# Kernel tuning notes

Hardware: AMD Instinct MI355X
Metric: run time of the kernel (lower is better)

The kernel has to match this reference:

```python
import jax, jax.numpy as jnp
import numpy as np

NUM_NODES = 200000
NUM_EDGES = 200000
NUM_GRAPHS = 2048
F_IN = 128
H = 64


def setup_inputs() -> dict:
    key = jax.random.key(0)
    ks = jax.random.split(key, 16)
    x = jax.random.normal(ks[0], (NUM_NODES, F_IN), dtype=jnp.float32)
    edge_index = jax.random.randint(ks[1], (2, NUM_EDGES), 0, NUM_NODES, dtype=jnp.int64)
    batch = jnp.sort(jax.random.randint(ks[2], (NUM_NODES,), 0, NUM_GRAPHS, dtype=jnp.int64))
    s_in = 1.0 / np.sqrt(F_IN)
    s_h = 1.0 / np.sqrt(H)
    W1a = jax.random.uniform(ks[3], (F_IN, H), jnp.float32, -s_in, s_in)
    b1a = jax.random.uniform(ks[4], (H,), jnp.float32, -s_in, s_in)
    W1b = jax.random.uniform(ks[5], (H, H), jnp.float32, -s_h, s_h)
    b1b = jax.random.uniform(ks[6], (H,), jnp.float32, -s_h, s_h)
    W2a = jax.random.uniform(ks[7], (H, H), jnp.float32, -s_h, s_h)
    b2a = jax.random.uniform(ks[8], (H,), jnp.float32, -s_h, s_h)
    W2b = jax.random.uniform(ks[9], (H, H), jnp.float32, -s_h, s_h)
    b2b = jax.random.uniform(ks[10], (H,), jnp.float32, -s_h, s_h)
    fcW = jax.random.uniform(ks[11], (H, 1), jnp.float32, -s_h, s_h)
    fcb = jax.random.uniform(ks[12], (1,), jnp.float32, -s_h, s_h)
    return {"x": x, "edge_index": edge_index, "batch": batch,
            "W1a": W1a, "b1a": b1a, "W1b": W1b, "b1b": b1b,
            "W2a": W2a, "b2a": b2a, "W2b": W2b, "b2b": b2b,
            "fcW": fcW, "fcb": fcb}


def gin_conv(h, edge_index, Wa, ba, Wb, bb):
    # sum aggregation: messages from source (row 0) scattered to target (row 1)
    msgs = h[edge_index[0]]  # [E, D]
    agg = jax.ops.segment_sum(msgs, edge_index[1], num_segments=NUM_NODES)
    z = h + agg  # eps = 0 default: (1+eps)*x + sum_j x_j
    z = jnp.maximum(z @ Wa + ba, 0.0)
    return z @ Wb + bb


def reference(x, edge_index, batch, W1a, b1a, W1b, b1b, W2a, b2a, W2b, b2b, fcW, fcb):
    h = jnp.maximum(gin_conv(x, edge_index, W1a, b1a, W1b, b1b), 0.0)
    h = jnp.maximum(gin_conv(h, edge_index, W2a, b2a, W2b, b2b), 0.0)
    # global mean pool per graph
    sums = jax.ops.segment_sum(h, batch, num_segments=NUM_GRAPHS)  # [G, H]
    counts = jax.ops.segment_sum(jnp.ones((h.shape[0],), h.dtype), batch, num_segments=NUM_GRAPHS)
    pooled = sums / jnp.maximum(counts, 1.0)[:, None]
    out = pooled @ fcW + fcb  # [G, 1]
    return out.squeeze(-1)
```

## Files before the change

kernel.cpp:

```cpp
#include <hip/hip_runtime.h>
#include <hip/hip_bf16.h>


#define NODES 200000
#define NPAD  200064
#define EDGES 200000
#define GRAPHS 2048
#define NB_SCAN 782

typedef __attribute__((ext_vector_type(8))) short short8;
typedef __attribute__((ext_vector_type(4))) float f32x4;

__device__ __forceinline__ unsigned short f2bf(float f) {
    unsigned u = __builtin_bit_cast(unsigned, f);
    u = (u + 0x7fffu + ((u >> 16) & 1u)) >> 16;
    return (unsigned short)u;
}
__device__ __forceinline__ float bf2f(unsigned short h) {
    unsigned u = ((unsigned)h) << 16;
    return __builtin_bit_cast(float, u);
}

__device__ __forceinline__ void wconv(const float* __restrict__ W,
                                      short* __restrict__ F, int e, int NE)
{
    int lane = e & 63, nb = (e >> 6) & 3, kc = e >> 8;
    int col = nb * 16 + (lane & 15);
    int kb = kc * 32 + ((lane >> 4) * 8);
    short8 hi, lo;
    #pragma unroll
    for (int j = 0; j < 8; ++j) {
        float w = W[(size_t)(kb + j) * 64 + col];
        unsigned short h = f2bf(w);
        float r = w - bf2f(h);
        hi[j] = (short)h;
        lo[j] = (short)f2bf(r);
    }
    *reinterpret_cast<short8*>(F + (size_t)e * 8) = hi;
    *reinterpret_cast<short8*>(F + (size_t)NE * 8 + (size_t)e * 8) = lo;
}

__global__ __launch_bounds__(256) void setup_k(
    const float* __restrict__ W1a, const float* __restrict__ W1b,
    const float* __restrict__ W2a, const float* __restrict__ W2b,
    short* __restrict__ F1a, short* __restrict__ F1b,
    short* __restrict__ F2a, short* __restrict__ F2b,
    int* __restrict__ cnt, float* __restrict__ gacc)
{
    int t = blockIdx.x * 256 + threadIdx.x;
    if (t < NODES) cnt[t] = 0;
    if (t < GRAPHS) gacc[t] = 0.f;
    if (t < 1024)      wconv(W1a, F1a, t, 1024);
    else if (t < 1536) wconv(W1b, F1b, t - 1024, 512);
    else if (t < 2048) wconv(W2a, F2a, t - 1536, 512);
    else if (t < 2560) wconv(W2b, F2b, t - 2048, 512);
}

__global__ __launch_bounds__(256) void count_k(
    const int* __restrict__ ei, int* __restrict__ cnt, int E)
{
    int e = blockIdx.x * 256 + threadIdx.x;
    if (e < E) atomicAdd(&cnt[ei[E + e]], 1);
}

__global__ __launch_bounds__(256) void scan1_k(
    const int* __restrict__ cnt, int* __restrict__ excl,
    int* __restrict__ bsum, int N)
{
    __shared__ int sh[256];
    int tid = threadIdx.x;
    int i = blockIdx.x * 256 + tid;
    int v = (i < N) ? cnt[i] : 0;
    sh[tid] = v;
    __syncthreads();
    for (int off = 1; off < 256; off <<= 1) {
        int t = (tid >= off) ? sh[tid - off] : 0;
        __syncthreads();
        sh[tid] += t;
        __syncthreads();
    }
    if (i < N) excl[i] = sh[tid] - v;
    if (tid == 255) bsum[blockIdx.x] = sh[255];
}

__global__ __launch_bounds__(256) void scan23_k(
    int* __restrict__ rowptr, const int* __restrict__ bsum,
    int* __restrict__ cursor, int N, int E)
{
    __shared__ int wsum[4];
    __shared__ int soff;
    int tid = threadIdx.x;
    int partial = 0;
    for (int b = tid; b < blockIdx.x; b += 256) partial += bsum[b];
    #pragma unroll
    for (int off = 32; off >= 1; off >>= 1) partial += __shfl_down(partial, off);
    if ((tid & 63) == 0) wsum[tid >> 6] = partial;
    __syncthreads();
    if (tid == 0) soff = wsum[0] + wsum[1] + wsum[2] + wsum[3];
    __syncthreads();
    int i = blockIdx.x * 256 + tid;
    if (i < N) {
        int v = rowptr[i] + soff;
        rowptr[i] = v;
        cursor[i] = v;
    }
    if (i == 0) rowptr[N] = E;
}

__global__ __launch_bounds__(256) void fill_k(
    const int* __restrict__ ei, int* __restrict__ cursor,
    int* __restrict__ srcs, int E)
{
    int e = blockIdx.x * 256 + threadIdx.x;
    if (e < E) {
        int d = ei[E + e];
        int p = atomicAdd(&cursor[d], 1);
        srcs[p] = ei[e];
    }
}

__device__ __forceinline__ void cvt_a8(const float4& a, const float4& b,
                                       short8& hi, short8& lo)
{
    float av[8] = {a.x, a.y, a.z, a.w, b.x, b.y, b.z, b.w};
    #pragma unroll
    for (int j = 0; j < 8; ++j) {
        unsigned short h = f2bf(av[j]);
        float r = av[j] - bf2f(h);
        hi[j] = (short)h;
        lo[j] = (short)f2bf(r);
    }
}

__global__ __launch_bounds__(256) void mm1_k(
    const float* __restrict__ A, const short* __restrict__ Wf,
    float* __restrict__ out, int N)
{
    const int tid = threadIdx.x;
    const int lane = tid & 63;
    const int wv = tid >> 6;
    const int row0w = blockIdx.x * 128 + wv * 32;
    const int grp = lane >> 4, c = lane & 15;
    const int koff = grp * 8;

    const float* Ar0 = A + (size_t)min(row0w + c, N - 1) * 128;
    const float* Ar1 = A + (size_t)min(row0w + 16 + c, N - 1) * 128;

    f32x4 acc[2][4];
    #pragma unroll
    for (int rg = 0; rg < 2; ++rg)
        #pragma unroll
        for (int nb = 0; nb < 4; ++nb)
            acc[rg][nb] = (f32x4){0.f, 0.f, 0.f, 0.f};

    #pragma unroll
    for (int kc = 0; kc < 4; ++kc) {
        const int kb = kc * 32 + koff;
        float4 a00 = *reinterpret_cast<const float4*>(Ar0 + kb);
        float4 a01 = *reinterpret_cast<const float4*>(Ar0 + kb + 4);
        float4 a10 = *reinterpret_cast<const float4*>(Ar1 + kb);
        float4 a11 = *reinterpret_cast<const float4*>(Ar1 + kb + 4);
        short8 h0, l0, h1, l1;
        cvt_a8(a00, a01, h0, l0);
        cvt_a8(a10, a11, h1, l1);
        #pragma unroll
        for (int nb = 0; nb < 4; ++nb) {
            short8 whi = *reinterpret_cast<const short8*>(Wf + ((size_t)((kc * 4 + nb) * 64) + lane) * 8);
            short8 wlo = *reinterpret_cast<const short8*>(Wf + ((size_t)(1024 + (kc * 4 + nb) * 64) + lane) * 8);
            acc[0][nb] = __builtin_amdgcn_mfma_f32_16x16x32_bf16(h0, whi, acc[0][nb], 0, 0, 0);
            acc[0][nb] = __builtin_amdgcn_mfma_f32_16x16x32_bf16(l0, whi, acc[0][nb], 0, 0, 0);
            acc[0][nb] = __builtin_amdgcn_mfma_f32_16x16x32_bf16(h0, wlo, acc[0][nb], 0, 0, 0);
            acc[1][nb] = __builtin_amdgcn_mfma_f32_16x16x32_bf16(h1, whi, acc[1][nb], 0, 0, 0);
            acc[1][nb] = __builtin_amdgcn_mfma_f32_16x16x32_bf16(l1, whi, acc[1][nb], 0, 0, 0);
            acc[1][nb] = __builtin_amdgcn_mfma_f32_16x16x32_bf16(h1, wlo, acc[1][nb], 0, 0, 0);
        }
    }

    #pragma unroll
    for (int rg = 0; rg < 2; ++rg)
        #pragma unroll
        for (int nb = 0; nb < 4; ++nb)
            #pragma unroll
            for (int reg = 0; reg < 4; ++reg)
                out[(size_t)(row0w + rg * 16 + grp * 4 + reg) * 64 + nb * 16 + c] = acc[rg][nb][reg];
}

__device__ __forceinline__ void agg_frag16(
    const float* __restrict__ y, const int* __restrict__ rowptr,
    const int* __restrict__ srcs, const float* __restrict__ bias,
    int n, int koff, bool valid, short8 fh[2], short8 fl[2])
{
    if (!valid) {
        #pragma unroll
        for (int i = 0; i < 8; ++i) {
            fh[0][i] = 0; fl[0][i] = 0; fh[1][i] = 0; fl[1][i] = 0;
        }
        return;
    }
    float a[16];
    {
        const float* yr = y + (size_t)n * 64;
        float4 a0 = *reinterpret_cast<const float4*>(yr + koff);
        float4 a1 = *reinterpret_cast<const float4*>(yr + koff + 4);
        float4 a2 = *reinterpret_cast<const float4*>(yr + 32 + koff);
        float4 a3 = *reinterpret_cast<const float4*>(yr + 32 + koff + 4);
        float4 b0 = *reinterpret_cast<const float4*>(bias + koff);
        float4 b1 = *reinterpret_cast<const float4*>(bias + koff + 4);
        float4 b2 = *reinterpret_cast<const float4*>(bias + 32 + koff);
        float4 b3 = *reinterpret_cast<const float4*>(bias + 32 + koff + 4);
        a[0] = a0.x + b0.x;  a[1] = a0.y + b0.y;  a[2] = a0.z + b0.z;  a[3] = a0.w + b0.w;
        a[4] = a1.x + b1.x;  a[5] = a1.y + b1.y;  a[6] = a1.z + b1.z;  a[7] = a1.w + b1.w;
        a[8] = a2.x + b2.x;  a[9] = a2.y + b2.y;  a[10] = a2.z + b2.z; a[11] = a2.w + b2.w;
        a[12] = a3.x + b3.x; a[13] = a3.y + b3.y; a[14] = a3.z + b3.z; a[15] = a3.w + b3.w;
    }
    int s0 = rowptr[n], s1 = rowptr[n + 1];
    int j = s0;
    for (; j + 2 <= s1; j += 2) {
        const float* ysA = y + (size_t)srcs[j] * 64;
        const float* ysB = y + (size_t)srcs[j + 1] * 64;
        float4 A0 = *reinterpret_cast<const float4*>(ysA + koff);
        float4 A1 = *reinterpret_cast<const float4*>(ysA + koff + 4);
        float4 A2 = *reinterpret_cast<const float4*>(ysA + 32 + koff);
        float4 A3 = *reinterpret_cast<const float4*>(ysA + 32 + koff + 4);
        float4 B0 = *reinterpret_cast<const float4*>(ysB + koff);
        float4 B1 = *reinterpret_cast<const float4*>(ysB + koff + 4);
        float4 B2 = *reinterpret_cast<const float4*>(ysB + 32 + koff);
        float4 B3 = *reinterpret_cast<const float4*>(ysB + 32 + koff + 4);
        a[0] += A0.x;  a[1] += A0.y;  a[2] += A0.z;  a[3] += A0.w;
        a[4] += A1.x;  a[5] += A1.y;  a[6] += A1.z;  a[7] += A1.w;
        a[8] += A2.x;  a[9] += A2.y;  a[10] += A2.z; a[11] += A2.w;
        a[12] += A3.x; a[13] += A3.y; a[14] += A3.z; a[15] += A3.w;
        a[0] += B0.x;  a[1] += B0.y;  a[2] += B0.z;  a[3] += B0.w;
        a[4] += B1.x;  a[5] += B1.y;  a[6] += B1.z;  a[7] += B1.w;
        a[8] += B2.x;  a[9] += B2.y;  a[10] += B2.z; a[11] += B2.w;
        a[12] += B3.x; a[13] += B3.y; a[14] += B3.z; a[15] += B3.w;
    }
    if (j < s1) {
        const float* ys = y + (size_t)srcs[j] * 64;
        float4 v0 = *reinterpret_cast<const float4*>(ys + koff);
        float4 v1 = *reinterpret_cast<const float4*>(ys + koff + 4);
        float4 v2 = *reinterpret_cast<const float4*>(ys + 32 + koff);
        float4 v3 = *reinterpret_cast<const float4*>(ys + 32 + koff + 4);
        a[0] += v0.x;  a[1] += v0.y;  a[2] += v0.z;  a[3] += v0.w;
        a[4] += v1.x;  a[5] += v1.y;  a[6] += v1.z;  a[7] += v1.w;
        a[8] += v2.x;  a[9] += v2.y;  a[10] += v2.z; a[11] += v2.w;
        a[12] += v3.x; a[13] += v3.y; a[14] += v3.z; a[15] += v3.w;
    }
    #pragma unroll
    for (int i = 0; i < 16; ++i) {
        float v = fmaxf(a[i], 0.f);
        unsigned short h = f2bf(v);
        float r = v - bf2f(h);
        fh[i >> 3][i & 7] = (short)h;
        fl[i >> 3][i & 7] = (short)f2bf(r);
    }
}

__global__ __launch_bounds__(256) void mmaggmm_k(
    const float* __restrict__ y, const int* __restrict__ rowptr,
    const int* __restrict__ srcs, const float* __restrict__ bagg,
    const short* __restrict__ Wf1, const float* __restrict__ b1,
    const short* __restrict__ Wf2, float* __restrict__ out, int N)
{
    __shared__ short hT[4][32 * 72];
    __shared__ short lT[4][32 * 72];
    const int tid = threadIdx.x;
    const int lane = tid & 63;
    const int wv = tid >> 6;
    const int row0w = blockIdx.x * 128 + wv * 32;
    const int grp = lane >> 4, c = lane & 15;
    const int koff = grp * 8;

    short8 fh0[2], fl0[2], fh1[2], fl1[2];
    {
        int n0 = row0w + c;
        int n1 = row0w + 16 + c;
        agg_frag16(y, rowptr, srcs, bagg, n0, koff, n0 < N, fh0, fl0);
        agg_frag16(y, rowptr, srcs, bagg, n1, koff, n1 < N, fh1, fl1);
    }

    f32x4 acc[2][4];
    #pragma unroll
    for (int rg = 0; rg < 2; ++rg)
        #pragma unroll
        for (int nb = 0; nb < 4; ++nb)
            acc[rg][nb] = (f32x4){0.f, 0.f, 0.f, 0.f};

    #pragma unroll
    for (int kc = 0; kc < 2; ++kc) {
        #pragma unroll
        for (int nb = 0; nb < 4; ++nb) {
            short8 whi = *reinterpret_cast<const short8*>(Wf1 + ((size_t)((kc * 4 + nb) * 64) + lane) * 8);
            short8 wlo = *reinterpret_cast<const short8*>(Wf1 + ((size_t)(512 + (kc * 4 + nb) * 64) + lane) * 8);
            acc[0][nb] = __builtin_amdgcn_mfma_f32_16x16x32_bf16(fh0[kc], whi, acc[0][nb], 0, 0, 0);
            acc[0][nb] = __builtin_amdgcn_mfma_f32_16x16x32_bf16(fl0[kc], whi, acc[0][nb], 0, 0, 0);
            acc[0][nb] = __builtin_amdgcn_mfma_f32_16x16x32_bf16(fh0[kc], wlo, acc[0][nb], 0, 0, 0);
            acc[1][nb] = __builtin_amdgcn_mfma_f32_16x16x32_bf16(fh1[kc], whi, acc[1][nb], 0, 0, 0);
            acc[1][nb] = __builtin_amdgcn_mfma_f32_16x16x32_bf16(fl1[kc], whi, acc[1][nb], 0, 0, 0);
            acc[1][nb] = __builtin_amdgcn_mfma_f32_16x16x32_bf16(fh1[kc], wlo, acc[1][nb], 0, 0, 0);
        }
    }

    #pragma unroll
    for (int rg = 0; rg < 2; ++rg)
        #pragma unroll
        for (int nb = 0; nb < 4; ++nb) {
            const int col = nb * 16 + c;
            const float bv = b1[col];
            #pragma unroll
            for (int reg = 0; reg < 4; ++reg) {
                const int lr = rg * 16 + grp * 4 + reg;
                float v = fmaxf(acc[rg][nb][reg] + bv, 0.f);
                unsigned short h = f2bf(v);
                float r = v - bf2f(h);
                hT[wv][lr * 72 + col] = (short)h;
                lT[wv][lr * 72 + col] = (short)f2bf(r);
            }
        }
    __syncthreads();

    f32x4 acc2[2][4];
    #pragma unroll
    for (int rg = 0; rg < 2; ++rg)
        #pragma unroll
        for (int nb = 0; nb < 4; ++nb)
            acc2[rg][nb] = (f32x4){0.f, 0.f, 0.f, 0.f};

    #pragma unroll
    for (int kc = 0; kc < 2; ++kc) {
        const int kb = kc * 32 + koff;
        short8 h0 = *reinterpret_cast<const short8*>(&hT[wv][(0 + c) * 72 + kb]);
        short8 l0 = *reinterpret_cast<const short8*>(&lT[wv][(0 + c) * 72 + kb]);
        short8 h1 = *reinterpret_cast<const short8*>(&hT[wv][(16 + c) * 72 + kb]);
        short8 l1 = *reinterpret_cast<const short8*>(&lT[wv][(16 + c) * 72 + kb]);
        #pragma unroll
        for (int nb = 0; nb < 4; ++nb) {
            short8 whi = *reinterpret_cast<const short8*>(Wf2 + ((size_t)((kc * 4 + nb) * 64) + lane) * 8);
            short8 wlo = *reinterpret_cast<const short8*>(Wf2 + ((size_t)(512 + (kc * 4 + nb) * 64) + lane) * 8);
            acc2[0][nb] = __builtin_amdgcn_mfma_f32_16x16x32_bf16(h0, whi, acc2[0][nb], 0, 0, 0);
            acc2[0][nb] = __builtin_amdgcn_mfma_f32_16x16x32_bf16(l0, whi, acc2[0][nb], 0, 0, 0);
            acc2[0][nb] = __builtin_amdgcn_mfma_f32_16x16x32_bf16(h0, wlo, acc2[0][nb], 0, 0, 0);
            acc2[1][nb] = __builtin_amdgcn_mfma_f32_16x16x32_bf16(h1, whi, acc2[1][nb], 0, 0, 0);
            acc2[1][nb] = __builtin_amdgcn_mfma_f32_16x16x32_bf16(l1, whi, acc2[1][nb], 0, 0, 0);
            acc2[1][nb] = __builtin_amdgcn_mfma_f32_16x16x32_bf16(h1, wlo, acc2[1][nb], 0, 0, 0);
        }
    }

    #pragma unroll
    for (int rg = 0; rg < 2; ++rg)
        #pragma unroll
        for (int nb = 0; nb < 4; ++nb)
            #pragma unroll
            for (int reg = 0; reg < 4; ++reg)
                out[(size_t)(row0w + rg * 16 + grp * 4 + reg) * 64 + nb * 16 + c] = acc2[rg][nb][reg];
}

__global__ __launch_bounds__(256) void mmaggpool_k(
    const float* __restrict__ y, const int* __restrict__ rowptr,
    const int* __restrict__ srcs, const float* __restrict__ bagg,
    const short* __restrict__ Wf, const float* __restrict__ bias,
    const float* __restrict__ fcW, const int* __restrict__ batch,
    float* __restrict__ gacc, int N)
{
    __shared__ float rd[4][32];
    __shared__ int bls[4][32];
    const int tid = threadIdx.x;
    const int lane = tid & 63;
    const int wv = tid >> 6;
    const int row0w = blockIdx.x * 128 + wv * 32;
    const int grp = lane >> 4, c = lane & 15;
    const int koff = grp * 8;

    if (lane < 32) bls[wv][lane] = batch[min(row0w + lane, N - 1)];

    short8 fh0[2], fl0[2], fh1[2], fl1[2];
    {
        int n0 = row0w + c;
        int n1 = row0w + 16 + c;
        agg_frag16(y, rowptr, srcs, bagg, n0, koff, n0 < N, fh0, fl0);
        agg_frag16(y, rowptr, srcs, bagg, n1, koff, n1 < N, fh1, fl1);
    }

    f32x4 acc[2][4];
    #pragma unroll
    for (int rg = 0; rg < 2; ++rg)
        #pragma unroll
        for (int nb = 0; nb < 4; ++nb)
            acc[rg][nb] = (f32x4){0.f, 0.f, 0.f, 0.f};

    #pragma unroll
    for (int kc = 0; kc < 2; ++kc) {
        #pragma unroll
        for (int nb = 0; nb < 4; ++nb) {
            short8 whi = *reinterpret_cast<const short8*>(Wf + ((size_t)((kc * 4 + nb) * 64) + lane) * 8);
            short8 wlo = *reinterpret_cast<const short8*>(Wf + ((size_t)(512 + (kc * 4 + nb) * 64) + lane) * 8);
            acc[0][nb] = __builtin_amdgcn_mfma_f32_16x16x32_bf16(fh0[kc], whi, acc[0][nb], 0, 0, 0);
            acc[0][nb] = __builtin_amdgcn_mfma_f32_16x16x32_bf16(fl0[kc], whi, acc[0][nb], 0, 0, 0);
            acc[0][nb] = __builtin_amdgcn_mfma_f32_16x16x32_bf16(fh0[kc], wlo, acc[0][nb], 0, 0, 0);
            acc[1][nb] = __builtin_amdgcn_mfma_f32_16x16x32_bf16(fh1[kc], whi, acc[1][nb], 0, 0, 0);
            acc[1][nb] = __builtin_amdgcn_mfma_f32_16x16x32_bf16(fl1[kc], whi, acc[1][nb], 0, 0, 0);
            acc[1][nb] = __builtin_amdgcn_mfma_f32_16x16x32_bf16(fh1[kc], wlo, acc[1][nb], 0, 0, 0);
        }
    }

    float bv[4], fw[4];
    #pragma unroll
    for (int nb = 0; nb < 4; ++nb) {
        bv[nb] = bias[nb * 16 + c];
        fw[nb] = fcW[nb * 16 + c];
    }

    #pragma unroll
    for (int rg = 0; rg < 2; ++rg)
        #pragma unroll
        for (int reg = 0; reg < 4; ++reg) {
            float t = 0.f;
            #pragma unroll
            for (int nb = 0; nb < 4; ++nb)
                t += fmaxf(acc[rg][nb][reg] + bv[nb], 0.f) * fw[nb];
            t += __shfl_xor(t, 1, 16);
            t += __shfl_xor(t, 2, 16);
            t += __shfl_xor(t, 4, 16);
            t += __shfl_xor(t, 8, 16);
            if (c == 0) rd[wv][rg * 16 + grp * 4 + reg] = t;
        }

    if (lane == 0) {
        int cnt = min(32, N - row0w);
        if (cnt > 0) {
            int curg = bls[wv][0];
            float s = rd[wv][0];
            for (int i = 1; i < cnt; ++i) {
                int g = bls[wv][i];
                float v = rd[wv][i];
                if (g == curg) s += v;
                else { atomicAdd(&gacc[curg], s); curg = g; s = v; }
            }
            atomicAdd(&gacc[curg], s);
        }
    }
}

__global__ __launch_bounds__(256) void finalize_k(
    const float* __restrict__ gacc, const int* __restrict__ batch,
    const float* __restrict__ fcb, float* __restrict__ out, int N, int G)
{
    int g = blockIdx.x * 256 + threadIdx.x;
    if (g >= G) return;
    int lo = 0, hi = N;
    while (lo < hi) { int m = (lo + hi) >> 1; if (batch[m] < g) lo = m + 1; else hi = m; }
    int start = lo;
    hi = N;
    while (lo < hi) { int m = (lo + hi) >> 1; if (batch[m] < g + 1) lo = m + 1; else hi = m; }
    float cnt = fmaxf((float)(lo - start), 1.f);
    out[g] = gacc[g] / cnt + fcb[0];
}

extern "C" void kernel_launch(void* const* d_in, const int* in_sizes, int n_in,
                              void* d_out, int out_size, void* d_ws, size_t ws_size,
                              hipStream_t stream)
{
    const float* x     = (const float*)d_in[0];
    const int*   ei    = (const int*)d_in[1];
    const int*   batch = (const int*)d_in[2];
    const float* W1a   = (const float*)d_in[3];
    const float* b1a   = (const float*)d_in[4];
    const float* W1b   = (const float*)d_in[5];
    const float* b1b   = (const float*)d_in[6];
    const float* W2a   = (const float*)d_in[7];
    const float* b2a   = (const float*)d_in[8];
    const float* W2b   = (const float*)d_in[9];
    const float* b2b   = (const float*)d_in[10];
    const float* fcW   = (const float*)d_in[11];
    const float* fcb   = (const float*)d_in[12];
    float* out = (float*)d_out;

    const int N = NODES, E = EDGES, G = GRAPHS;
    char* ws = (char*)d_ws;

    float* y1 = (float*)ws;
    float* y2 = (float*)(ws + (size_t)NPAD * 64 * 4);
    char*  rest = ws + 2 * (size_t)NPAD * 64 * 4;
    int* cnt    = (int*)rest;
    int* rowptr = cnt + NODES;
    int* cursor = rowptr + NODES + 1;
    int* srcs   = cursor + NODES;
    int* bsum   = srcs + EDGES;
    float* gacc = (float*)(bsum + NB_SCAN + 2);
    short* F1a  = (short*)(((size_t)(gacc + GRAPHS) + 63) & ~(size_t)63);
    short* F1b  = F1a + 2 * 1024 * 8;
    short* F2a  = F1b + 2 * 512 * 8;
    short* F2b  = F2a + 2 * 512 * 8;

    const int NBLK = NPAD / 128;

    setup_k<<<NB_SCAN, 256, 0, stream>>>(W1a, W1b, W2a, W2b, F1a, F1b, F2a, F2b, cnt, gacc);
    count_k<<<NB_SCAN, 256, 0, stream>>>(ei, cnt, E);
    scan1_k<<<NB_SCAN, 256, 0, stream>>>(cnt, rowptr, bsum, N);
    scan23_k<<<NB_SCAN, 256, 0, stream>>>(rowptr, bsum, cursor, N, E);
    fill_k<<<NB_SCAN, 256, 0, stream>>>(ei, cursor, srcs, E);

    mm1_k<<<NBLK, 256, 0, stream>>>(x, F1a, y1, N);

    mmaggmm_k<<<NBLK, 256, 0, stream>>>(y1, rowptr, srcs, b1a, F1b, b1b, F2a, y2, N);

    mmaggpool_k<<<NBLK, 256, 0, stream>>>(y2, rowptr, srcs, b2a, F2b, b2b, fcW, batch, gacc, N);
    finalize_k<<<(G + 255) / 256, 256, 0, stream>>>(gacc, batch, fcb, out, N, G);
}
```

Baseline: 290.7 us.

## Merge CSR build kernels into one cooperative kernel with grid syncs

Replaces the five separate setup, count, scan and fill launches with a single cooperative kernel that separates the phases with grid-wide barriers. This removes four kernel launches and their inter-kernel gaps in the preprocessing stage. It requires all 782 blocks to be co-resident, and grid.sync barriers carry their own cost, which could offset the savings on launch overhead.

```diff
diff --git a/kernel.cpp b/kernel.cpp
--- a/kernel.cpp
+++ b/kernel.cpp
@@ -1,5 +1,8 @@
 #include <hip/hip_runtime.h>
 #include <hip/hip_bf16.h>
+#include <hip/hip_cooperative_groups.h>
+
+namespace cg = cooperative_groups;
 
 
 #define NODES 200000
@@ -40,82 +43,70 @@
     *reinterpret_cast<short8*>(F + (size_t)NE * 8 + (size_t)e * 8) = lo;
 }
 
-__global__ __launch_bounds__(256) void setup_k(
+__global__ __launch_bounds__(256) void csr_k(
+    const int* __restrict__ ei,
     const float* __restrict__ W1a, const float* __restrict__ W1b,
     const float* __restrict__ W2a, const float* __restrict__ W2b,
     short* __restrict__ F1a, short* __restrict__ F1b,
     short* __restrict__ F2a, short* __restrict__ F2b,
-    int* __restrict__ cnt, float* __restrict__ gacc)
-{
-    int t = blockIdx.x * 256 + threadIdx.x;
+    int* __restrict__ cnt, int* __restrict__ rowptr, int* __restrict__ cursor,
+    int* __restrict__ srcs, int* __restrict__ bsum, float* __restrict__ gacc)
+{
+    cg::grid_group grid = cg::this_grid();
+    const int tid = threadIdx.x;
+    const int t = blockIdx.x * 256 + tid;
+
     if (t < NODES) cnt[t] = 0;
     if (t < GRAPHS) gacc[t] = 0.f;
     if (t < 1024)      wconv(W1a, F1a, t, 1024);
     else if (t < 1536) wconv(W1b, F1b, t - 1024, 512);
     else if (t < 2048) wconv(W2a, F2a, t - 1536, 512);
     else if (t < 2560) wconv(W2b, F2b, t - 2048, 512);
-}
-
-__global__ __launch_bounds__(256) void count_k(
-    const int* __restrict__ ei, int* __restrict__ cnt, int E)
-{
-    int e = blockIdx.x * 256 + threadIdx.x;
-    if (e < E) atomicAdd(&cnt[ei[E + e]], 1);
-}
-
-__global__ __launch_bounds__(256) void scan1_k(
-    const int* __restrict__ cnt, int* __restrict__ excl,
-    int* __restrict__ bsum, int N)
-{
+    grid.sync();
+
+    if (t < EDGES) atomicAdd(&cnt[ei[EDGES + t]], 1);
+    grid.sync();
+
     __shared__ int sh[256];
-    int tid = threadIdx.x;
-    int i = blockIdx.x * 256 + tid;
-    int v = (i < N) ? cnt[i] : 0;
-    sh[tid] = v;
-    __syncthreads();
-    for (int off = 1; off < 256; off <<= 1) {
-        int t = (tid >= off) ? sh[tid - off] : 0;
+    {
+        int v = (t < NODES) ? cnt[t] : 0;
+        sh[tid] = v;
         __syncthreads();
-        sh[tid] += t;
+        for (int off = 1; off < 256; off <<= 1) {
+            int tmp = (tid >= off) ? sh[tid - off] : 0;
+            __syncthreads();
+            sh[tid] += tmp;
+            __syncthreads();
+        }
+        if (t < NODES) rowptr[t] = sh[tid] - v;
+        if (tid == 255) bsum[blockIdx.x] = sh[255];
+    }
+    grid.sync();
+
+    {
+        __shared__ int wsum[4];
+        __shared__ int soff;
+        int partial = 0;
+        for (int b = tid; b < blockIdx.x; b += 256) partial += bsum[b];
+        #pragma unroll
+        for (int off = 32; off >= 1; off >>= 1) partial += __shfl_down(partial, off);
+        if ((tid & 63) == 0) wsum[tid >> 6] = partial;
         __syncthreads();
-    }
-    if (i < N) excl[i] = sh[tid] - v;
-    if (tid == 255) bsum[blockIdx.x] = sh[255];
-}
-
-__global__ __launch_bounds__(256) void scan23_k(
-    int* __restrict__ rowptr, const int* __restrict__ bsum,
-    int* __restrict__ cursor, int N, int E)
-{
-    __shared__ int wsum[4];
-    __shared__ int soff;
-    int tid = threadIdx.x;
-    int partial = 0;
-    for (int b = tid; b < blockIdx.x; b += 256) partial += bsum[b];
-    #pragma unroll
-    for (int off = 32; off >= 1; off >>= 1) partial += __shfl_down(partial, off);
-    if ((tid & 63) == 0) wsum[tid >> 6] = partial;
-    __syncthreads();
-    if (tid == 0) soff = wsum[0] + wsum[1] + wsum[2] + wsum[3];
-    __syncthreads();
-    int i = blockIdx.x * 256 + tid;
-    if (i < N) {
-        int v = rowptr[i] + soff;
-        rowptr[i] = v;
-        cursor[i] = v;
-    }
-    if (i == 0) rowptr[N] = E;
-}
-
-__global__ __launch_bounds__(256) void fill_k(
-    const int* __restrict__ ei, int* __restrict__ cursor,
-    int* __restrict__ srcs, int E)
-{
-    int e = blockIdx.x * 256 + threadIdx.x;
-    if (e < E) {
-        int d = ei[E + e];
+        if (tid == 0) soff = wsum[0] + wsum[1] + wsum[2] + wsum[3];
+        __syncthreads();
+        if (t < NODES) {
+            int r = rowptr[t] + soff;
+            rowptr[t] = r;
+            cursor[t] = r;
+        }
+        if (t == 0) rowptr[NODES] = EDGES;
+    }
+    grid.sync();
+
+    if (t < EDGES) {
+        int d = ei[EDGES + t];
         int p = atomicAdd(&cursor[d], 1);
-        srcs[p] = ei[e];
+        srcs[p] = ei[t];
     }
 }
 
@@ -475,7 +466,7 @@
     const float* fcb   = (const float*)d_in[12];
     float* out = (float*)d_out;
 
-    const int N = NODES, E = EDGES, G = GRAPHS;
+    const int N = NODES, G = GRAPHS;
     char* ws = (char*)d_ws;
 
     float* y1 = (float*)ws;
@@ -494,11 +485,17 @@
 
     const int NBLK = NPAD / 128;
 
-    setup_k<<<NB_SCAN, 256, 0, stream>>>(W1a, W1b, W2a, W2b, F1a, F1b, F2a, F2b, cnt, gacc);
-    count_k<<<NB_SCAN, 256, 0, stream>>>(ei, cnt, E);
-    scan1_k<<<NB_SCAN, 256, 0, stream>>>(cnt, rowptr, bsum, N);
-    scan23_k<<<NB_SCAN, 256, 0, stream>>>(rowptr, bsum, cursor, N, E);
-    fill_k<<<NB_SCAN, 256, 0, stream>>>(ei, cursor, srcs, E);
+    {
+        void* args[] = {
+            (void*)&ei,
+            (void*)&W1a, (void*)&W1b, (void*)&W2a, (void*)&W2b,
+            (void*)&F1a, (void*)&F1b, (void*)&F2a, (void*)&F2b,
+            (void*)&cnt, (void*)&rowptr, (void*)&cursor,
+            (void*)&srcs, (void*)&bsum, (void*)&gacc
+        };
+        hipLaunchCooperativeKernel((const void*)csr_k, dim3(NB_SCAN), dim3(256),
+                                   args, 0, stream);
+    }
 
     mm1_k<<<NBLK, 256, 0, stream>>>(x, F1a, y1, N);
 
```

Measured after the change: 613.5 us. +111.0%, slower.
